# Kernel optimization log

Hardware: AMD Instinct MI355X
Metric: run time of the kernel (lower is better)

The kernel has to match this reference:

```python
import jax, jax.numpy as jnp
import numpy as np

N_USER = 100000
N_ITEM = 100000
E = 500000
IN, HID, OUT = 128, 128, 64
ETYPES = ["rates", "rated_by", "follows", "similar"]
# canonical etypes: (user,rates,item), (item,rated_by,user), (user,follows,user), (item,similar,item)
SRC_N = {"rates": N_USER, "rated_by": N_ITEM, "follows": N_USER, "similar": N_ITEM}
DST_N = {"rates": N_ITEM, "rated_by": N_USER, "follows": N_USER, "similar": N_ITEM}


def setup_inputs() -> dict:
    key = jax.random.key(0)
    ks = iter(jax.random.split(key, 64))
    inp = {}
    inp["emb_user"] = jax.random.normal(next(ks), (N_USER, IN), jnp.float32)
    inp["emb_item"] = jax.random.normal(next(ks), (N_ITEM, IN), jnp.float32)
    for et in ETYPES:
        inp[f"W1_{et}"] = jax.random.normal(next(ks), (IN, HID), jnp.float32) / np.float32(np.sqrt(IN))
        inp[f"b1_{et}"] = jnp.zeros((HID,), jnp.float32)
        inp[f"W2_{et}"] = jax.random.normal(next(ks), (HID, OUT), jnp.float32) / np.float32(np.sqrt(HID))
        inp[f"b2_{et}"] = jnp.zeros((OUT,), jnp.float32)
    for et in ETYPES:
        inp[f"src_{et}"] = jax.random.randint(next(ks), (E,), 0, SRC_N[et], jnp.int32)
        inp[f"dst_{et}"] = jax.random.randint(next(ks), (E,), 0, DST_N[et], jnp.int32)
    return inp


def _mean_agg(Wh, src, dst, n_dst):
    """copy_u('Wh','m') + mean('m','h') for one relation."""
    m = jnp.take(Wh, src, axis=0)                                   # [E, d] gather
    s = jax.ops.segment_sum(m, dst, num_segments=n_dst)             # [n_dst, d]
    cnt = jax.ops.segment_sum(jnp.ones(src.shape, Wh.dtype), dst, num_segments=n_dst)
    return s / jnp.maximum(cnt, 1.0)[:, None]                       # zero-indegree -> 0


def _layer(xu, xi, Wr, br, Wrb, brb, Wf, bf, Ws, bs,
           s_r, d_r, s_rb, d_rb, s_f, d_f, s_s, d_s):
    # cross-etype 'sum' reducer
    h_user = (_mean_agg(xi @ Wrb + brb, s_rb, d_rb, N_USER)
              + _mean_agg(xu @ Wf + bf, s_f, d_f, N_USER))
    h_item = (_mean_agg(xu @ Wr + br, s_r, d_r, N_ITEM)
              + _mean_agg(xi @ Ws + bs, s_s, d_s, N_ITEM))
    return h_user, h_item


def reference(emb_user, emb_item,
              W1_rates, b1_rates, W1_rated_by, b1_rated_by, W1_follows, b1_follows, W1_similar, b1_similar,
              W2_rates, b2_rates, W2_rated_by, b2_rated_by, W2_follows, b2_follows, W2_similar, b2_similar,
              src_rates, dst_rates, src_rated_by, dst_rated_by,
              src_follows, dst_follows, src_similar, dst_similar):
    hu, hi = _layer(emb_user, emb_item,
                    W1_rates, b1_rates, W1_rated_by, b1_rated_by,
                    W1_follows, b1_follows, W1_similar, b1_similar,
                    src_rates, dst_rates, src_rated_by, dst_rated_by,
                    src_follows, dst_follows, src_similar, dst_similar)
    hu = jax.nn.leaky_relu(hu)  # torch F.leaky_relu default slope 0.01
    hi = jax.nn.leaky_relu(hi)
    ou, oi = _layer(hu, hi,
                    W2_rates, b2_rates, W2_rated_by, b2_rated_by,
                    W2_follows, b2_follows, W2_similar, b2_similar,
                    src_rates, dst_rates, src_rated_by, dst_rated_by,
                    src_follows, dst_follows, src_similar, dst_similar)
    return ou  # ret_obj == 'user'
```

## Files before the change

kernel.cpp:

```cpp
#include <hip/hip_runtime.h>
#include <hip/hip_fp16.h>

#define N_USER 100000
#define N_ITEM 100000
#define NEDGE  500000
#define NKEY   400000
#define BSHIFT 11
#define NB     196
#define BCAP   11264
#define TILE   4096

typedef _Float16 f16x8 __attribute__((ext_vector_type(8)));
typedef float    f32x4 __attribute__((ext_vector_type(4)));

__global__ void prep_w(const float* __restrict__ W, __half* __restrict__ dst, int N)
{
    int i = blockIdx.x * 256 + threadIdx.x;
    if (i >= 128 * N) return;
    int k = i / N, n = i % N;
    int chunk = (n >> 4) * 4 + (k >> 5);
    int lane  = ((k >> 3) & 3) * 16 + (n & 15);
    int e     = k & 7;
    dst[(chunk * 64 + lane) * 8 + e] = __float2half(W[i]);
}

__global__ __launch_bounds__(256, 2)
void gemm2(const float* __restrict__ A,
           const __half* __restrict__ Wf0, const __half* __restrict__ Wf1,
           const float* __restrict__ b0, const float* __restrict__ b1,
           __half* __restrict__ out0, __half* __restrict__ out1, int M)
{
    const int tid = threadIdx.x;
    const int wave = tid >> 6, lane = tid & 63;
    const int l16 = lane & 15, lk = lane >> 4;
    const int rowBase = blockIdx.x * 128 + wave * 32;

    f32x4 acc0[2][8], acc1[2][8];
#pragma unroll
    for (int m = 0; m < 2; ++m)
#pragma unroll
        for (int n = 0; n < 8; ++n) { acc0[m][n] = (f32x4)0.f; acc1[m][n] = (f32x4)0.f; }

#pragma unroll
    for (int kt = 0; kt < 4; ++kt) {
        f16x8 af[2];
#pragma unroll
        for (int m = 0; m < 2; ++m) {
            int gr = rowBase + m * 16 + l16;
            float4 v0 = make_float4(0.f, 0.f, 0.f, 0.f), v1 = v0;
            if (gr < M) {
                const float* p = &A[(size_t)gr * 128 + kt * 32 + lk * 8];
                v0 = *reinterpret_cast<const float4*>(p);
                v1 = *reinterpret_cast<const float4*>(p + 4);
            }
            f16x8 a;
            a[0] = (_Float16)v0.x; a[1] = (_Float16)v0.y;
            a[2] = (_Float16)v0.z; a[3] = (_Float16)v0.w;
            a[4] = (_Float16)v1.x; a[5] = (_Float16)v1.y;
            a[6] = (_Float16)v1.z; a[7] = (_Float16)v1.w;
            af[m] = a;
        }
#pragma unroll
        for (int n = 0; n < 8; ++n) {
            const size_t cidx = (size_t)((n * 4 + kt) * 64 + lane) * 8;
            f16x8 bf0 = *reinterpret_cast<const f16x8*>(Wf0 + cidx);
            f16x8 bf1 = *reinterpret_cast<const f16x8*>(Wf1 + cidx);
            acc0[0][n] = __builtin_amdgcn_mfma_f32_16x16x32_f16(af[0], bf0, acc0[0][n], 0, 0, 0);
            acc0[1][n] = __builtin_amdgcn_mfma_f32_16x16x32_f16(af[1], bf0, acc0[1][n], 0, 0, 0);
            acc1[0][n] = __builtin_amdgcn_mfma_f32_16x16x32_f16(af[0], bf1, acc1[0][n], 0, 0, 0);
            acc1[1][n] = __builtin_amdgcn_mfma_f32_16x16x32_f16(af[1], bf1, acc1[1][n], 0, 0, 0);
        }
    }

#pragma unroll
    for (int m = 0; m < 2; ++m) {
        int gr0 = rowBase + m * 16 + lk * 4;
#pragma unroll
        for (int n = 0; n < 8; ++n) {
            float bv0 = b0[n * 16 + l16];
            float bv1 = b1[n * 16 + l16];
#pragma unroll
            for (int r = 0; r < 4; ++r) {
                int gr = gr0 + r;
                if (gr < M) {
                    out0[(size_t)gr * 128 + n * 16 + l16] = __float2half(acc0[m][n][r] + bv0);
                    out1[(size_t)gr * 128 + n * 16 + l16] = __float2half(acc1[m][n][r] + bv1);
                }
            }
        }
    }
}

__global__ __launch_bounds__(256, 4)
void gemm1_l2(const __half* __restrict__ A, const __half* __restrict__ Wf,
              const float* __restrict__ bias, __half* __restrict__ out, int M)
{
    const int tid = threadIdx.x;
    const int wave = tid >> 6, lane = tid & 63;
    const int l16 = lane & 15, lk = lane >> 4;
    const int rowBase = blockIdx.x * 128 + wave * 32;

    f32x4 acc[2][4];
#pragma unroll
    for (int m = 0; m < 2; ++m)
#pragma unroll
        for (int n = 0; n < 4; ++n) acc[m][n] = (f32x4)0.f;

#pragma unroll
    for (int kt = 0; kt < 4; ++kt) {
        f16x8 af[2];
#pragma unroll
        for (int m = 0; m < 2; ++m) {
            int gr = rowBase + m * 16 + l16;
            f16x8 a = (f16x8)(_Float16)0.f;
            if (gr < M)
                a = *reinterpret_cast<const f16x8*>(&A[(size_t)gr * 128 + kt * 32 + lk * 8]);
#pragma unroll
            for (int e = 0; e < 8; ++e) {
                float x = (float)a[e];
                x = x > 0.f ? x : 0.01f * x;
                a[e] = (_Float16)x;
            }
            af[m] = a;
        }
#pragma unroll
        for (int n = 0; n < 4; ++n) {
            const size_t cidx = (size_t)((n * 4 + kt) * 64 + lane) * 8;
            f16x8 bf = *reinterpret_cast<const f16x8*>(Wf + cidx);
            acc[0][n] = __builtin_amdgcn_mfma_f32_16x16x32_f16(af[0], bf, acc[0][n], 0, 0, 0);
            acc[1][n] = __builtin_amdgcn_mfma_f32_16x16x32_f16(af[1], bf, acc[1][n], 0, 0, 0);
        }
    }

#pragma unroll
    for (int m = 0; m < 2; ++m) {
        int gr0 = rowBase + m * 16 + lk * 4;
#pragma unroll
        for (int n = 0; n < 4; ++n) {
            float bv = bias[n * 16 + l16];
#pragma unroll
            for (int r = 0; r < 4; ++r) {
                int gr = gr0 + r;
                if (gr < M)
                    out[(size_t)gr * 64 + n * 16 + l16] = __float2half(acc[m][n][r] + bv);
            }
        }
    }
}

__global__ __launch_bounds__(256)
void partition_kernel(const int* __restrict__ s0, const int* __restrict__ d0,
                      const int* __restrict__ s1, const int* __restrict__ d1,
                      const int* __restrict__ s2, const int* __restrict__ d2,
                      const int* __restrict__ s3, const int* __restrict__ d3,
                      int* __restrict__ bucket_cursor, uint2* __restrict__ pairbuf)
{
    __shared__ int cntS[256], lscan[256], gbase[256], cur[256];
    __shared__ uint2 stage[TILE];
    __shared__ unsigned char bslot[TILE];

    const int t = threadIdx.x;
    const int rel = blockIdx.y;
    const int* S = rel == 0 ? s0 : rel == 1 ? s1 : rel == 2 ? s2 : s3;
    const int* D = rel == 0 ? d0 : rel == 1 ? d1 : rel == 2 ? d2 : d3;
    const int tileBase = blockIdx.x * TILE;
    const int tileN = min(TILE, NEDGE - tileBase);

    cntS[t] = 0;
    __syncthreads();

    int key[16], sv[16];
#pragma unroll
    for (int k = 0; k < 16; ++k) {
        int i = tileBase + k * 256 + t;
        if (i < NEDGE) {
            sv[k]  = S[i];
            key[k] = rel * 100000 + D[i];
            atomicAdd(&cntS[key[k] >> BSHIFT], 1);
        } else key[k] = -1;
    }
    __syncthreads();

    const int c = cntS[t];
    lscan[t] = c;
    __syncthreads();
    for (int off = 1; off < 256; off <<= 1) {
        int v = (t >= off) ? lscan[t - off] : 0;
        __syncthreads();
        lscan[t] += v;
        __syncthreads();
    }
    const int ex = lscan[t] - c;
    __syncthreads();
    lscan[t] = ex;
    cur[t]   = ex;
    if (t < NB && c > 0) gbase[t] = atomicAdd(&bucket_cursor[t], c);
    __syncthreads();

#pragma unroll
    for (int k = 0; k < 16; ++k) {
        if (key[k] >= 0) {
            int b = key[k] >> BSHIFT;
            int slot = atomicAdd(&cur[b], 1);
            stage[slot] = make_uint2((unsigned)key[k], (unsigned)sv[k]);
            bslot[slot] = (unsigned char)b;
        }
    }
    __syncthreads();

    for (int j = t; j < tileN; j += 256) {
        int b = bslot[j];
        pairbuf[(size_t)b * BCAP + gbase[b] + (j - lscan[b])] = stage[j];
    }
}

__global__ __launch_bounds__(256)
void bucket_scan(const int* __restrict__ bucket_cursor, int* __restrict__ gstart,
                 int* __restrict__ row_start)
{
    __shared__ int sd[256];
    int t = threadIdx.x;
    int v = (t < NB) ? bucket_cursor[t] : 0;
    sd[t] = v;
    __syncthreads();
    for (int off = 1; off < 256; off <<= 1) {
        int u = (t >= off) ? sd[t - off] : 0;
        __syncthreads();
        sd[t] += u;
        __syncthreads();
    }
    if (t < NB) gstart[t] = sd[t] - v;
    if (t == NB) gstart[NB] = sd[NB - 1];
    if (t == 0)  row_start[NKEY] = 4 * NEDGE;
}

__global__ __launch_bounds__(256)
void build_csr(const uint2* __restrict__ pairbuf, const int* __restrict__ bucket_cursor,
               const int* __restrict__ gstart, int* __restrict__ row_start,
               int* __restrict__ csr_src)
{
    __shared__ int hist[2048];
    __shared__ int scan2[2048];
    __shared__ int partial[256];

    const int b = blockIdx.x;
    const int t = threadIdx.x;
    const int cnt = bucket_cursor[b];
    const int gs  = gstart[b];
    const uint2* pb = pairbuf + (size_t)b * BCAP;
    const int keyBase = b << BSHIFT;
    const int nbin = min(2048, NKEY - keyBase);

    for (int k = t; k < 2048; k += 256) hist[k] = 0;
    __syncthreads();
    for (int j = t; j < cnt; j += 256)
        atomicAdd(&hist[(int)pb[j].x - keyBase], 1);
    __syncthreads();

    const int base8 = t * 8;
    int s = 0;
#pragma unroll
    for (int k = 0; k < 8; ++k) s += hist[base8 + k];
    partial[t] = s;
    __syncthreads();
    for (int off = 1; off < 256; off <<= 1) {
        int u = (t >= off) ? partial[t - off] : 0;
        __syncthreads();
        partial[t] += u;
        __syncthreads();
    }
    int run = partial[t] - s;
#pragma unroll
    for (int k = 0; k < 8; ++k) { scan2[base8 + k] = run; run += hist[base8 + k]; }
    __syncthreads();

    for (int k = t; k < nbin; k += 256) row_start[keyBase + k] = gs + scan2[k];
    for (int k = t; k < 2048; k += 256) hist[k] = scan2[k];
    __syncthreads();

    for (int j = t; j < cnt; j += 256) {
        uint2 p = pb[j];
        int pos = atomicAdd(&hist[(int)p.x - keyBase], 1);
        csr_src[gs + pos] = (int)p.y;
    }
}

template<int D, bool ACCUM, bool HOUT>
__global__ __launch_bounds__(256)
void pull_kernel(const __half* __restrict__ Wh, const int* __restrict__ row_start,
                 const int* __restrict__ csr_src, void* __restrict__ outv,
                 int segBase, int nRows)
{
    int wid = (blockIdx.x * blockDim.x + threadIdx.x) >> 6;
    int lane = threadIdx.x & 63;
    if (wid >= nRows) return;
    int idx = segBase + wid;
    int start = row_start[idx];
    int end   = row_start[idx + 1];
    float inv = 1.0f / (float)max(end - start, 1);
    int sub = lane >> 5;
    int sl  = lane & 31;

    if (D == 128) {
        float4 acc = make_float4(0.f, 0.f, 0.f, 0.f);
        int e = start;
        for (; e + 4 <= end; e += 4) {
            int sA = csr_src[e + sub];
            int sB = csr_src[e + 2 + sub];
            uint2 uA = *reinterpret_cast<const uint2*>(&Wh[(size_t)sA * 128 + sl * 4]);
            uint2 uB = *reinterpret_cast<const uint2*>(&Wh[(size_t)sB * 128 + sl * 4]);
            float2 fa0 = __half22float2(*reinterpret_cast<__half2*>(&uA.x));
            float2 fa1 = __half22float2(*reinterpret_cast<__half2*>(&uA.y));
            float2 fb0 = __half22float2(*reinterpret_cast<__half2*>(&uB.x));
            float2 fb1 = __half22float2(*reinterpret_cast<__half2*>(&uB.y));
            acc.x += fa0.x + fb0.x; acc.y += fa0.y + fb0.y;
            acc.z += fa1.x + fb1.x; acc.w += fa1.y + fb1.y;
        }
        if (e + 2 <= end) {
            int s = csr_src[e + sub];
            uint2 u = *reinterpret_cast<const uint2*>(&Wh[(size_t)s * 128 + sl * 4]);
            float2 f0 = __half22float2(*reinterpret_cast<__half2*>(&u.x));
            float2 f1 = __half22float2(*reinterpret_cast<__half2*>(&u.y));
            acc.x += f0.x; acc.y += f0.y; acc.z += f1.x; acc.w += f1.y;
            e += 2;
        }
        if (e < end && sub == 0) {
            int s = csr_src[e];
            uint2 u = *reinterpret_cast<const uint2*>(&Wh[(size_t)s * 128 + sl * 4]);
            float2 f0 = __half22float2(*reinterpret_cast<__half2*>(&u.x));
            float2 f1 = __half22float2(*reinterpret_cast<__half2*>(&u.y));
            acc.x += f0.x; acc.y += f0.y; acc.z += f1.x; acc.w += f1.y;
        }
        acc.x += __shfl_xor(acc.x, 32);
        acc.y += __shfl_xor(acc.y, 32);
        acc.z += __shfl_xor(acc.z, 32);
        acc.w += __shfl_xor(acc.w, 32);
        if (sub == 0) {
            acc.x *= inv; acc.y *= inv; acc.z *= inv; acc.w *= inv;
            if constexpr (HOUT) {
                __half* o = (__half*)outv + (size_t)wid * 128 + sl * 4;
                if (ACCUM) {
                    uint2 cur = *reinterpret_cast<const uint2*>(o);
                    float2 c0 = __half22float2(*reinterpret_cast<__half2*>(&cur.x));
                    float2 c1 = __half22float2(*reinterpret_cast<__half2*>(&cur.y));
                    acc.x += c0.x; acc.y += c0.y; acc.z += c1.x; acc.w += c1.y;
                }
                uint2 st;
                *reinterpret_cast<__half2*>(&st.x) = __floats2half2_rn(acc.x, acc.y);
                *reinterpret_cast<__half2*>(&st.y) = __floats2half2_rn(acc.z, acc.w);
                *reinterpret_cast<uint2*>(o) = st;
            } else {
                float* o = (float*)outv + (size_t)wid * 128 + sl * 4;
                float4* p = reinterpret_cast<float4*>(o);
                if (ACCUM) {
                    float4 c = *p;
                    c.x += acc.x; c.y += acc.y; c.z += acc.z; c.w += acc.w;
                    *p = c;
                } else {
                    *p = acc;
                }
            }
        }
    } else {
        float2 acc = make_float2(0.f, 0.f);
        int e = start;
        for (; e + 4 <= end; e += 4) {
            int sA = csr_src[e + sub];
            int sB = csr_src[e + 2 + sub];
            float2 fA = __half22float2(*reinterpret_cast<const __half2*>(&Wh[(size_t)sA * 64 + sl * 2]));
            float2 fB = __half22float2(*reinterpret_cast<const __half2*>(&Wh[(size_t)sB * 64 + sl * 2]));
            acc.x += fA.x + fB.x; acc.y += fA.y + fB.y;
        }
        if (e + 2 <= end) {
            int s = csr_src[e + sub];
            float2 f = __half22float2(*reinterpret_cast<const __half2*>(&Wh[(size_t)s * 64 + sl * 2]));
            acc.x += f.x; acc.y += f.y;
            e += 2;
        }
        if (e < end && sub == 0) {
            int s = csr_src[e];
            float2 f = __half22float2(*reinterpret_cast<const __half2*>(&Wh[(size_t)s * 64 + sl * 2]));
            acc.x += f.x; acc.y += f.y;
        }
        acc.x += __shfl_xor(acc.x, 32);
        acc.y += __shfl_xor(acc.y, 32);
        if (sub == 0) {
            acc.x *= inv; acc.y *= inv;
            if constexpr (HOUT) {
                __half* o = (__half*)outv + (size_t)wid * 64 + sl * 2;
                if (ACCUM) {
                    __half2 cur = *reinterpret_cast<const __half2*>(o);
                    float2 c = __half22float2(cur);
                    acc.x += c.x; acc.y += c.y;
                }
                *reinterpret_cast<__half2*>(o) = __floats2half2_rn(acc.x, acc.y);
            } else {
                float2* p = reinterpret_cast<float2*>((float*)outv + (size_t)wid * 64 + sl * 2);
                if (ACCUM) {
                    float2 c = *p;
                    c.x += acc.x; c.y += acc.y;
                    *p = c;
                } else {
                    *p = make_float2(acc.x, acc.y);
                }
            }
        }
    }
}

extern "C" void kernel_launch(void* const* d_in, const int* in_sizes, int n_in,
                              void* d_out, int out_size, void* d_ws, size_t ws_size,
                              hipStream_t stream)
{
    const float* emb_user = (const float*)d_in[0];
    const float* emb_item = (const float*)d_in[1];
    const float* W1_rates    = (const float*)d_in[2];
    const float* b1_rates    = (const float*)d_in[3];
    const float* W1_rated_by = (const float*)d_in[6];
    const float* b1_rated_by = (const float*)d_in[7];
    const float* W2_rated_by = (const float*)d_in[8];
    const float* b2_rated_by = (const float*)d_in[9];
    const float* W1_follows  = (const float*)d_in[10];
    const float* b1_follows  = (const float*)d_in[11];
    const float* W2_follows  = (const float*)d_in[12];
    const float* b2_follows  = (const float*)d_in[13];
    const float* W1_similar  = (const float*)d_in[14];
    const float* b1_similar  = (const float*)d_in[15];
    const int* src_rates    = (const int*)d_in[18];
    const int* dst_rates    = (const int*)d_in[19];
    const int* src_rated_by = (const int*)d_in[20];
    const int* dst_rated_by = (const int*)d_in[21];
    const int* src_follows  = (const int*)d_in[22];
    const int* dst_follows  = (const int*)d_in[23];
    const int* src_similar  = (const int*)d_in[24];
    const int* dst_similar  = (const int*)d_in[25];

    float* out = (float*)d_out;

    char* base = (char*)d_ws;
    __half* WhX  = (__half*)base;
    __half* WhY  = (__half*)(base + 25600000);
    __half* accI = (__half*)(base + 51200000);
    __half* accU = (__half*)(base + 76800000);
    int* csr_src   = (int*)(base + 102400000);
    int* row_start = (int*)(base + 110400000);
    int* bucket_cursor = (int*)(base + 112000016);
    int* gstart        = (int*)(base + 112001056);
    __half* wf = (__half*)(base + 112002080);
    __half* wf_rates    = wf;
    __half* wf_follows  = wf + 16384;
    __half* wf_similar  = wf + 32768;
    __half* wf_rated_by = wf + 49152;
    __half* wf2_rb      = wf + 65536;
    __half* wf2_f       = wf + 73728;
    uint2* pairbuf = (uint2*)WhX;

    const int SEG_RATES    = 0;
    const int SEG_RATED_BY = 100000;
    const int SEG_FOLLOWS  = 200000;
    const int SEG_SIMILAR  = 300000;

    hipMemsetAsync(bucket_cursor, 0, 256 * sizeof(int), stream);

    prep_w<<<64, 256, 0, stream>>>(W1_rates,    wf_rates,    128);
    prep_w<<<64, 256, 0, stream>>>(W1_follows,  wf_follows,  128);
    prep_w<<<64, 256, 0, stream>>>(W1_similar,  wf_similar,  128);
    prep_w<<<64, 256, 0, stream>>>(W1_rated_by, wf_rated_by, 128);
    prep_w<<<32, 256, 0, stream>>>(W2_rated_by, wf2_rb, 64);
    prep_w<<<32, 256, 0, stream>>>(W2_follows,  wf2_f,  64);

    const int tiles = (NEDGE + TILE - 1) / TILE;
    partition_kernel<<<dim3(tiles, 4), 256, 0, stream>>>(
        src_rates, dst_rates, src_rated_by, dst_rated_by,
        src_follows, dst_follows, src_similar, dst_similar,
        bucket_cursor, pairbuf);
    bucket_scan<<<1, 256, 0, stream>>>(bucket_cursor, gstart, row_start);
    build_csr<<<NB, 256, 0, stream>>>(pairbuf, bucket_cursor, gstart, row_start, csr_src);

    const int gb = (100000 + 127) / 128;
    const int pb = (100000 * 64 + 255) / 256;

    gemm2<<<gb, 256, 0, stream>>>(emb_user, wf_rates, wf_follows, b1_rates, b1_follows,
                                  WhX, WhY, N_USER);
    pull_kernel<128, false, true><<<pb, 256, 0, stream>>>(WhX, row_start, csr_src, accI, SEG_RATES, N_ITEM);
    pull_kernel<128, false, true><<<pb, 256, 0, stream>>>(WhY, row_start, csr_src, accU, SEG_FOLLOWS, N_USER);
    gemm2<<<gb, 256, 0, stream>>>(emb_item, wf_similar, wf_rated_by, b1_similar, b1_rated_by,
                                  WhX, WhY, N_ITEM);
    pull_kernel<128, true, true><<<pb, 256, 0, stream>>>(WhX, row_start, csr_src, accI, SEG_SIMILAR, N_ITEM);
    pull_kernel<128, true, true><<<pb, 256, 0, stream>>>(WhY, row_start, csr_src, accU, SEG_RATED_BY, N_USER);

    gemm1_l2<<<gb, 256, 0, stream>>>(accI, wf2_rb, b2_rated_by, WhX, N_ITEM);
    pull_kernel<64, false, false><<<pb, 256, 0, stream>>>(WhX, row_start, csr_src, out, SEG_RATED_BY, N_USER);
    gemm1_l2<<<gb, 256, 0, stream>>>(accU, wf2_f, b2_follows, WhY, N_USER);
    pull_kernel<64, true, false><<<pb, 256, 0, stream>>>(WhY, row_start, csr_src, out, SEG_FOLLOWS, N_USER);
}
```

Before: 382.1 us.

## Batch relation kernels into paired launches and widen per-lane gather loads

Merges the six weight-prep launches into one 2D grid and pairs the two per-relation pull kernels and the two layer-2 GEMMs into single launches using blockIdx.y. The 128-wide pull now has each lane load 16 bytes, with four edge groups per wave reduced by shuffles. The final 64-wide output step is fused into one kernel that sums both relations and writes the float output once, with no read-modify-write. gemm2 drops to 16 rows per wave to free registers for higher occupancy, in exchange for loading each weight fragment once per 16 rows instead of once per 32.

```diff
diff --git a/kernel.cpp b/kernel.cpp
--- a/kernel.cpp
+++ b/kernel.cpp
@@ -10,11 +10,25 @@
 #define BCAP   11264
 #define TILE   4096
 
+#define SEG_RATES    0
+#define SEG_RATED_BY 100000
+#define SEG_FOLLOWS  200000
+#define SEG_SIMILAR  300000
+
 typedef _Float16 f16x8 __attribute__((ext_vector_type(8)));
 typedef float    f32x4 __attribute__((ext_vector_type(4)));
 
-__global__ void prep_w(const float* __restrict__ W, __half* __restrict__ dst, int N)
-{
+__global__ void prep_w_all(const float* __restrict__ W0, const float* __restrict__ W1,
+                           const float* __restrict__ W2, const float* __restrict__ W3,
+                           const float* __restrict__ W4, const float* __restrict__ W5,
+                           __half* __restrict__ D0, __half* __restrict__ D1,
+                           __half* __restrict__ D2, __half* __restrict__ D3,
+                           __half* __restrict__ D4, __half* __restrict__ D5)
+{
+    int y = blockIdx.y;
+    const float* W = y == 0 ? W0 : y == 1 ? W1 : y == 2 ? W2 : y == 3 ? W3 : y == 4 ? W4 : W5;
+    __half* dst    = y == 0 ? D0 : y == 1 ? D1 : y == 2 ? D2 : y == 3 ? D3 : y == 4 ? D4 : D5;
+    int N = y < 4 ? 128 : 64;
     int i = blockIdx.x * 256 + threadIdx.x;
     if (i >= 128 * N) return;
     int k = i / N, n = i % N;
@@ -24,7 +38,7 @@
     dst[(chunk * 64 + lane) * 8 + e] = __float2half(W[i]);
 }
 
-__global__ __launch_bounds__(256, 2)
+__global__ __launch_bounds__(256, 3)
 void gemm2(const float* __restrict__ A,
            const __half* __restrict__ Wf0, const __half* __restrict__ Wf1,
            const float* __restrict__ b0, const float* __restrict__ b1,
@@ -33,68 +47,70 @@
     const int tid = threadIdx.x;
     const int wave = tid >> 6, lane = tid & 63;
     const int l16 = lane & 15, lk = lane >> 4;
-    const int rowBase = blockIdx.x * 128 + wave * 32;
-
-    f32x4 acc0[2][8], acc1[2][8];
-#pragma unroll
-    for (int m = 0; m < 2; ++m)
-#pragma unroll
-        for (int n = 0; n < 8; ++n) { acc0[m][n] = (f32x4)0.f; acc1[m][n] = (f32x4)0.f; }
-
+    const int rowBase = blockIdx.x * 64 + wave * 16;
+
+    f32x4 acc0[8], acc1[8];
+#pragma unroll
+    for (int n = 0; n < 8; ++n) { acc0[n] = (f32x4)0.f; acc1[n] = (f32x4)0.f; }
+
+    const int gr = rowBase + l16;
+    const bool valid = gr < M;
+    const float* ap = A + (size_t)(valid ? gr : 0) * 128 + lk * 8;
+    float4 av[8];
 #pragma unroll
     for (int kt = 0; kt < 4; ++kt) {
-        f16x8 af[2];
-#pragma unroll
-        for (int m = 0; m < 2; ++m) {
-            int gr = rowBase + m * 16 + l16;
-            float4 v0 = make_float4(0.f, 0.f, 0.f, 0.f), v1 = v0;
-            if (gr < M) {
-                const float* p = &A[(size_t)gr * 128 + kt * 32 + lk * 8];
-                v0 = *reinterpret_cast<const float4*>(p);
-                v1 = *reinterpret_cast<const float4*>(p + 4);
-            }
-            f16x8 a;
-            a[0] = (_Float16)v0.x; a[1] = (_Float16)v0.y;
-            a[2] = (_Float16)v0.z; a[3] = (_Float16)v0.w;
-            a[4] = (_Float16)v1.x; a[5] = (_Float16)v1.y;
-            a[6] = (_Float16)v1.z; a[7] = (_Float16)v1.w;
-            af[m] = a;
-        }
+        av[2 * kt]     = *reinterpret_cast<const float4*>(ap + kt * 32);
+        av[2 * kt + 1] = *reinterpret_cast<const float4*>(ap + kt * 32 + 4);
+    }
+    if (!valid) {
+#pragma unroll
+        for (int j = 0; j < 8; ++j) av[j] = make_float4(0.f, 0.f, 0.f, 0.f);
+    }
+
+#pragma unroll
+    for (int kt = 0; kt < 4; ++kt) {
+        f16x8 af;
+        af[0] = (_Float16)av[2 * kt].x;     af[1] = (_Float16)av[2 * kt].y;
+        af[2] = (_Float16)av[2 * kt].z;     af[3] = (_Float16)av[2 * kt].w;
+        af[4] = (_Float16)av[2 * kt + 1].x; af[5] = (_Float16)av[2 * kt + 1].y;
+        af[6] = (_Float16)av[2 * kt + 1].z; af[7] = (_Float16)av[2 * kt + 1].w;
 #pragma unroll
         for (int n = 0; n < 8; ++n) {
             const size_t cidx = (size_t)((n * 4 + kt) * 64 + lane) * 8;
             f16x8 bf0 = *reinterpret_cast<const f16x8*>(Wf0 + cidx);
             f16x8 bf1 = *reinterpret_cast<const f16x8*>(Wf1 + cidx);
-            acc0[0][n] = __builtin_amdgcn_mfma_f32_16x16x32_f16(af[0], bf0, acc0[0][n], 0, 0, 0);
-            acc0[1][n] = __builtin_amdgcn_mfma_f32_16x16x32_f16(af[1], bf0, acc0[1][n], 0, 0, 0);
-            acc1[0][n] = __builtin_amdgcn_mfma_f32_16x16x32_f16(af[0], bf1, acc1[0][n], 0, 0, 0);
-            acc1[1][n] = __builtin_amdgcn_mfma_f32_16x16x32_f16(af[1], bf1, acc1[1][n], 0, 0, 0);
-        }
-    }
-
-#pragma unroll
-    for (int m = 0; m < 2; ++m) {
-        int gr0 = rowBase + m * 16 + lk * 4;
-#pragma unroll
-        for (int n = 0; n < 8; ++n) {
-            float bv0 = b0[n * 16 + l16];
-            float bv1 = b1[n * 16 + l16];
-#pragma unroll
-            for (int r = 0; r < 4; ++r) {
-                int gr = gr0 + r;
-                if (gr < M) {
-                    out0[(size_t)gr * 128 + n * 16 + l16] = __float2half(acc0[m][n][r] + bv0);
-                    out1[(size_t)gr * 128 + n * 16 + l16] = __float2half(acc1[m][n][r] + bv1);
-                }
+            acc0[n] = __builtin_amdgcn_mfma_f32_16x16x32_f16(af, bf0, acc0[n], 0, 0, 0);
+            acc1[n] = __builtin_amdgcn_mfma_f32_16x16x32_f16(af, bf1, acc1[n], 0, 0, 0);
+        }
+    }
+
+    const int gr0 = rowBase + lk * 4;
+#pragma unroll
+    for (int n = 0; n < 8; ++n) {
+        float bv0 = b0[n * 16 + l16];
+        float bv1 = b1[n * 16 + l16];
+#pragma unroll
+        for (int r = 0; r < 4; ++r) {
+            int grr = gr0 + r;
+            if (grr < M) {
+                out0[(size_t)grr * 128 + n * 16 + l16] = __float2half(acc0[n][r] + bv0);
+                out1[(size_t)grr * 128 + n * 16 + l16] = __float2half(acc1[n][r] + bv1);
             }
         }
     }
 }
 
 __global__ __launch_bounds__(256, 4)
-void gemm1_l2(const __half* __restrict__ A, const __half* __restrict__ Wf,
-              const float* __restrict__ bias, __half* __restrict__ out, int M)
-{
+void gemm1_l2_pair(const __half* __restrict__ A0, const __half* __restrict__ A1,
+                   const __half* __restrict__ Wf0, const __half* __restrict__ Wf1,
+                   const float* __restrict__ bias0, const float* __restrict__ bias1,
+                   __half* __restrict__ O0, __half* __restrict__ O1, int M)
+{
+    const __half* A  = blockIdx.y ? A1 : A0;
+    const __half* Wf = blockIdx.y ? Wf1 : Wf0;
+    const float* bias = blockIdx.y ? bias1 : bias0;
+    __half* out = blockIdx.y ? O1 : O0;
+
     const int tid = threadIdx.x;
     const int wave = tid >> 6, lane = tid & 63;
     const int l16 = lane & 15, lk = lane >> 4;
@@ -285,126 +301,101 @@
     }
 }
 
-template<int D, bool ACCUM, bool HOUT>
+template<bool ACCUM>
 __global__ __launch_bounds__(256)
-void pull_kernel(const __half* __restrict__ Wh, const int* __restrict__ row_start,
-                 const int* __restrict__ csr_src, void* __restrict__ outv,
-                 int segBase, int nRows)
-{
-    int wid = (blockIdx.x * blockDim.x + threadIdx.x) >> 6;
-    int lane = threadIdx.x & 63;
-    if (wid >= nRows) return;
-    int idx = segBase + wid;
-    int start = row_start[idx];
-    int end   = row_start[idx + 1];
-    float inv = 1.0f / (float)max(end - start, 1);
-    int sub = lane >> 5;
-    int sl  = lane & 31;
-
-    if (D == 128) {
-        float4 acc = make_float4(0.f, 0.f, 0.f, 0.f);
-        int e = start;
-        for (; e + 4 <= end; e += 4) {
-            int sA = csr_src[e + sub];
-            int sB = csr_src[e + 2 + sub];
-            uint2 uA = *reinterpret_cast<const uint2*>(&Wh[(size_t)sA * 128 + sl * 4]);
-            uint2 uB = *reinterpret_cast<const uint2*>(&Wh[(size_t)sB * 128 + sl * 4]);
-            float2 fa0 = __half22float2(*reinterpret_cast<__half2*>(&uA.x));
-            float2 fa1 = __half22float2(*reinterpret_cast<__half2*>(&uA.y));
-            float2 fb0 = __half22float2(*reinterpret_cast<__half2*>(&uB.x));
-            float2 fb1 = __half22float2(*reinterpret_cast<__half2*>(&uB.y));
-            acc.x += fa0.x + fb0.x; acc.y += fa0.y + fb0.y;
-            acc.z += fa1.x + fb1.x; acc.w += fa1.y + fb1.y;
-        }
-        if (e + 2 <= end) {
-            int s = csr_src[e + sub];
-            uint2 u = *reinterpret_cast<const uint2*>(&Wh[(size_t)s * 128 + sl * 4]);
-            float2 f0 = __half22float2(*reinterpret_cast<__half2*>(&u.x));
-            float2 f1 = __half22float2(*reinterpret_cast<__half2*>(&u.y));
-            acc.x += f0.x; acc.y += f0.y; acc.z += f1.x; acc.w += f1.y;
-            e += 2;
-        }
-        if (e < end && sub == 0) {
-            int s = csr_src[e];
-            uint2 u = *reinterpret_cast<const uint2*>(&Wh[(size_t)s * 128 + sl * 4]);
-            float2 f0 = __half22float2(*reinterpret_cast<__half2*>(&u.x));
-            float2 f1 = __half22float2(*reinterpret_cast<__half2*>(&u.y));
-            acc.x += f0.x; acc.y += f0.y; acc.z += f1.x; acc.w += f1.y;
-        }
-        acc.x += __shfl_xor(acc.x, 32);
-        acc.y += __shfl_xor(acc.y, 32);
-        acc.z += __shfl_xor(acc.z, 32);
-        acc.w += __shfl_xor(acc.w, 32);
-        if (sub == 0) {
-            acc.x *= inv; acc.y *= inv; acc.z *= inv; acc.w *= inv;
-            if constexpr (HOUT) {
-                __half* o = (__half*)outv + (size_t)wid * 128 + sl * 4;
-                if (ACCUM) {
-                    uint2 cur = *reinterpret_cast<const uint2*>(o);
-                    float2 c0 = __half22float2(*reinterpret_cast<__half2*>(&cur.x));
-                    float2 c1 = __half22float2(*reinterpret_cast<__half2*>(&cur.y));
-                    acc.x += c0.x; acc.y += c0.y; acc.z += c1.x; acc.w += c1.y;
-                }
-                uint2 st;
-                *reinterpret_cast<__half2*>(&st.x) = __floats2half2_rn(acc.x, acc.y);
-                *reinterpret_cast<__half2*>(&st.y) = __floats2half2_rn(acc.z, acc.w);
-                *reinterpret_cast<uint2*>(o) = st;
-            } else {
-                float* o = (float*)outv + (size_t)wid * 128 + sl * 4;
-                float4* p = reinterpret_cast<float4*>(o);
-                if (ACCUM) {
-                    float4 c = *p;
-                    c.x += acc.x; c.y += acc.y; c.z += acc.z; c.w += acc.w;
-                    *p = c;
-                } else {
-                    *p = acc;
-                }
+void pull128_pair(const __half* __restrict__ WhA, int segA, __half* __restrict__ outA,
+                  const __half* __restrict__ WhB, int segB, __half* __restrict__ outB,
+                  const int* __restrict__ row_start, const int* __restrict__ csr_src)
+{
+    const __half* Wh = blockIdx.y ? WhB : WhA;
+    __half* out      = blockIdx.y ? outB : outA;
+    const int seg    = blockIdx.y ? segB : segA;
+
+    const int wid = (blockIdx.x * 256 + threadIdx.x) >> 6;
+    if (wid >= 100000) return;
+    const int g  = (threadIdx.x >> 4) & 3;
+    const int sl = threadIdx.x & 15;
+    const int idx = seg + wid;
+    const int s0 = row_start[idx], s1 = row_start[idx + 1];
+    const float inv = 1.0f / (float)max(s1 - s0, 1);
+
+    float acc[8];
+#pragma unroll
+    for (int j = 0; j < 8; ++j) acc[j] = 0.f;
+
+    for (int e = s0 + g; e < s1; e += 4) {
+        int src = csr_src[e];
+        uint4 u = *reinterpret_cast<const uint4*>(&Wh[(size_t)src * 128 + sl * 8]);
+        const __half2* hp = reinterpret_cast<const __half2*>(&u);
+#pragma unroll
+        for (int j = 0; j < 4; ++j) {
+            float2 f = __half22float2(hp[j]);
+            acc[2 * j] += f.x; acc[2 * j + 1] += f.y;
+        }
+    }
+#pragma unroll
+    for (int j = 0; j < 8; ++j) {
+        acc[j] += __shfl_xor(acc[j], 16);
+        acc[j] += __shfl_xor(acc[j], 32);
+        acc[j] *= inv;
+    }
+    if (g == 0) {
+        __half* o = out + (size_t)wid * 128 + sl * 8;
+        if (ACCUM) {
+            uint4 c = *reinterpret_cast<const uint4*>(o);
+            const __half2* cp = reinterpret_cast<const __half2*>(&c);
+#pragma unroll
+            for (int j = 0; j < 4; ++j) {
+                float2 f = __half22float2(cp[j]);
+                acc[2 * j] += f.x; acc[2 * j + 1] += f.y;
             }
         }
-    } else {
-        float2 acc = make_float2(0.f, 0.f);
-        int e = start;
-        for (; e + 4 <= end; e += 4) {
-            int sA = csr_src[e + sub];
-            int sB = csr_src[e + 2 + sub];
-            float2 fA = __half22float2(*reinterpret_cast<const __half2*>(&Wh[(size_t)sA * 64 + sl * 2]));
-            float2 fB = __half22float2(*reinterpret_cast<const __half2*>(&Wh[(size_t)sB * 64 + sl * 2]));
-            acc.x += fA.x + fB.x; acc.y += fA.y + fB.y;
-        }
-        if (e + 2 <= end) {
-            int s = csr_src[e + sub];
-            float2 f = __half22float2(*reinterpret_cast<const __half2*>(&Wh[(size_t)s * 64 + sl * 2]));
-            acc.x += f.x; acc.y += f.y;
-            e += 2;
-        }
-        if (e < end && sub == 0) {
-            int s = csr_src[e];
-            float2 f = __half22float2(*reinterpret_cast<const __half2*>(&Wh[(size_t)s * 64 + sl * 2]));
-            acc.x += f.x; acc.y += f.y;
-        }
-        acc.x += __shfl_xor(acc.x, 32);
-        acc.y += __shfl_xor(acc.y, 32);
-        if (sub == 0) {
-            acc.x *= inv; acc.y *= inv;
-            if constexpr (HOUT) {
-                __half* o = (__half*)outv + (size_t)wid * 64 + sl * 2;
-                if (ACCUM) {
-                    __half2 cur = *reinterpret_cast<const __half2*>(o);
-                    float2 c = __half22float2(cur);
-                    acc.x += c.x; acc.y += c.y;
-                }
-                *reinterpret_cast<__half2*>(o) = __floats2half2_rn(acc.x, acc.y);
-            } else {
-                float2* p = reinterpret_cast<float2*>((float*)outv + (size_t)wid * 64 + sl * 2);
-                if (ACCUM) {
-                    float2 c = *p;
-                    c.x += acc.x; c.y += acc.y;
-                    *p = c;
-                } else {
-                    *p = make_float2(acc.x, acc.y);
-                }
-            }
-        }
+        uint4 st;
+        __half2* sp = reinterpret_cast<__half2*>(&st);
+#pragma unroll
+        for (int j = 0; j < 4; ++j) sp[j] = __floats2half2_rn(acc[2 * j], acc[2 * j + 1]);
+        *reinterpret_cast<uint4*>(o) = st;
+    }
+}
+
+__global__ __launch_bounds__(256)
+void dual_pull64(const __half* __restrict__ WhRB, const __half* __restrict__ WhF,
+                 const int* __restrict__ row_start, const int* __restrict__ csr_src,
+                 float* __restrict__ out)
+{
+    const int wid = (blockIdx.x * 256 + threadIdx.x) >> 6;
+    if (wid >= N_USER) return;
+    const int g  = (threadIdx.x >> 4) & 3;
+    const int sl = threadIdx.x & 15;
+
+    const int rb0 = row_start[SEG_RATED_BY + wid], rb1 = row_start[SEG_RATED_BY + wid + 1];
+    const int f0  = row_start[SEG_FOLLOWS  + wid], f1  = row_start[SEG_FOLLOWS  + wid + 1];
+    const float invRB = 1.0f / (float)max(rb1 - rb0, 1);
+    const float invF  = 1.0f / (float)max(f1 - f0, 1);
+
+    const __half* Wh = (g < 2) ? WhRB : WhF;
+    const int e0 = (g < 2) ? rb0 + (g & 1) : f0 + (g & 1);
+    const int e1 = (g < 2) ? rb1 : f1;
+
+    float acc[4] = {0.f, 0.f, 0.f, 0.f};
+    for (int e = e0; e < e1; e += 2) {
+        int src = csr_src[e];
+        uint2 u = *reinterpret_cast<const uint2*>(&Wh[(size_t)src * 64 + sl * 4]);
+        const __half2* hp = reinterpret_cast<const __half2*>(&u);
+        float2 fa = __half22float2(hp[0]);
+        float2 fb = __half22float2(hp[1]);
+        acc[0] += fa.x; acc[1] += fa.y; acc[2] += fb.x; acc[3] += fb.y;
+    }
+    const float sc = (g < 2) ? invRB : invF;
+#pragma unroll
+    for (int j = 0; j < 4; ++j) {
+        acc[j] += __shfl_xor(acc[j], 16);
+        acc[j] *= sc;
+        acc[j] += __shfl_xor(acc[j], 32);
+    }
+    if (g == 0) {
+        float4 v = make_float4(acc[0], acc[1], acc[2], acc[3]);
+        *reinterpret_cast<float4*>(&out[(size_t)wid * 64 + sl * 4]) = v;
     }
 }
 
@@ -455,19 +446,11 @@
     __half* wf2_f       = wf + 73728;
     uint2* pairbuf = (uint2*)WhX;
 
-    const int SEG_RATES    = 0;
-    const int SEG_RATED_BY = 100000;
-    const int SEG_FOLLOWS  = 200000;
-    const int SEG_SIMILAR  = 300000;
-
     hipMemsetAsync(bucket_cursor, 0, 256 * sizeof(int), stream);
 
-    prep_w<<<64, 256, 0, stream>>>(W1_rates,    wf_rates,    128);
-    prep_w<<<64, 256, 0, stream>>>(W1_follows,  wf_follows,  128);
-    prep_w<<<64, 256, 0, stream>>>(W1_similar,  wf_similar,  128);
-    prep_w<<<64, 256, 0, stream>>>(W1_rated_by, wf_rated_by, 128);
-    prep_w<<<32, 256, 0, stream>>>(W2_rated_by, wf2_rb, 64);
-    prep_w<<<32, 256, 0, stream>>>(W2_follows,  wf2_f,  64);
+    prep_w_all<<<dim3(64, 6), 256, 0, stream>>>(
+        W1_rates, W1_follows, W1_similar, W1_rated_by, W2_rated_by, W2_follows,
+        wf_rates, wf_follows, wf_similar, wf_rated_by, wf2_rb, wf2_f);
 
     const int tiles = (NEDGE + TILE - 1) / TILE;
     partition_kernel<<<dim3(tiles, 4), 256, 0, stream>>>(
@@ -477,20 +460,20 @@
     bucket_scan<<<1, 256, 0, stream>>>(bucket_cursor, gstart, row_start);
     build_csr<<<NB, 256, 0, stream>>>(pairbuf, bucket_cursor, gstart, row_start, csr_src);
 
-    const int gb = (100000 + 127) / 128;
-    const int pb = (100000 * 64 + 255) / 256;
-
-    gemm2<<<gb, 256, 0, stream>>>(emb_user, wf_rates, wf_follows, b1_rates, b1_follows,
-                                  WhX, WhY, N_USER);
-    pull_kernel<128, false, true><<<pb, 256, 0, stream>>>(WhX, row_start, csr_src, accI, SEG_RATES, N_ITEM);
-    pull_kernel<128, false, true><<<pb, 256, 0, stream>>>(WhY, row_start, csr_src, accU, SEG_FOLLOWS, N_USER);
-    gemm2<<<gb, 256, 0, stream>>>(emb_item, wf_similar, wf_rated_by, b1_similar, b1_rated_by,
-                                  WhX, WhY, N_ITEM);
-    pull_kernel<128, true, true><<<pb, 256, 0, stream>>>(WhX, row_start, csr_src, accI, SEG_SIMILAR, N_ITEM);
-    pull_kernel<128, true, true><<<pb, 256, 0, stream>>>(WhY, row_start, csr_src, accU, SEG_RATED_BY, N_USER);
-
-    gemm1_l2<<<gb, 256, 0, stream>>>(accI, wf2_rb, b2_rated_by, WhX, N_ITEM);
-    pull_kernel<64, false, false><<<pb, 256, 0, stream>>>(WhX, row_start, csr_src, out, SEG_RATED_BY, N_USER);
-    gemm1_l2<<<gb, 256, 0, stream>>>(accU, wf2_f, b2_follows, WhY, N_USER);
-    pull_kernel<64, true, false><<<pb, 256, 0, stream>>>(WhY, row_start, csr_src, out, SEG_FOLLOWS, N_USER);
-}
+    const int gb2 = (100000 + 63) / 64;
+    const int gbl = (100000 + 127) / 128;
+    const int pb  = (100000 + 3) / 4;
+
+    gemm2<<<gb2, 256, 0, stream>>>(emb_user, wf_rates, wf_follows, b1_rates, b1_follows,
+                                   WhX, WhY, N_USER);
+    pull128_pair<false><<<dim3(pb, 2), 256, 0, stream>>>(
+        WhX, SEG_RATES, accI, WhY, SEG_FOLLOWS, accU, row_start, csr_src);
+    gemm2<<<gb2, 256, 0, stream>>>(emb_item, wf_similar, wf_rated_by, b1_similar, b1_rated_by,
+                                   WhX, WhY, N_ITEM);
+    pull128_pair<true><<<dim3(pb, 2), 256, 0, stream>>>(
+        WhX, SEG_SIMILAR, accI, WhY, SEG_RATED_BY, accU, row_start, csr_src);
+
+    gemm1_l2_pair<<<dim3(gbl, 2), 256, 0, stream>>>(
+        accI, accU, wf2_rb, wf2_f, b2_rated_by, b2_follows, WhX, WhY, N_ITEM);
+    dual_pull64<<<pb, 256, 0, stream>>>(WhX, WhY, row_start, csr_src, out);
+}
```

Measured after the change: 331.6 us. -13.2%, faster.
